# Kernel tuning notes

Measured on AMD Instinct MI355X. Metric: run time of the kernel, lower is better.

Reference implementation:

```python
import jax, jax.numpy as jnp
import numpy as np

N_LAYERS = 12
N_HEADS = 12
D_MODEL = 768
VOCAB = 50257
T_WIN = 1024
B, T = 4, 1024
STD = 0.02


def setup_inputs() -> dict:
    key = jax.random.key(0)
    ks = jax.random.split(key, 8)
    inp = jax.random.randint(ks[0], (B, T), 0, VOCAB)
    target = jax.random.randint(ks[1], (B, T), 0, VOCAB)
    wte = jax.random.normal(ks[2], (VOCAB, D_MODEL), jnp.float32) * STD
    wpe = jax.random.normal(ks[3], (T_WIN, D_MODEL), jnp.float32) * STD
    attn_w = jax.random.normal(ks[4], (N_LAYERS, D_MODEL, 3 * D_MODEL), jnp.float32) * STD
    proj_w = jax.random.normal(ks[5], (N_LAYERS, D_MODEL, D_MODEL), jnp.float32) * STD
    fc_w = jax.random.normal(ks[6], (N_LAYERS, D_MODEL, 4 * D_MODEL), jnp.float32) * STD
    fc2_w = jax.random.normal(ks[7], (N_LAYERS, 4 * D_MODEL, D_MODEL), jnp.float32) * STD
    return {
        'inp': inp, 'target': target, 'wte': wte, 'wpe': wpe,
        'ln1_w': jnp.ones((N_LAYERS, D_MODEL), jnp.float32),
        'ln1_b': jnp.zeros((N_LAYERS, D_MODEL), jnp.float32),
        'attn_w': attn_w,
        'attn_b': jnp.zeros((N_LAYERS, 3 * D_MODEL), jnp.float32),
        'proj_w': proj_w,
        'proj_b': jnp.zeros((N_LAYERS, D_MODEL), jnp.float32),
        'ln2_w': jnp.ones((N_LAYERS, D_MODEL), jnp.float32),
        'ln2_b': jnp.zeros((N_LAYERS, D_MODEL), jnp.float32),
        'fc_w': fc_w,
        'fc_b': jnp.zeros((N_LAYERS, 4 * D_MODEL), jnp.float32),
        'fc2_w': fc2_w,
        'fc2_b': jnp.zeros((N_LAYERS, D_MODEL), jnp.float32),
        'lnf_w': jnp.ones((D_MODEL,), jnp.float32),
        'lnf_b': jnp.zeros((D_MODEL,), jnp.float32),
    }


def _layernorm(x, w, b, eps=1e-5):
    mu = jnp.mean(x, axis=-1, keepdims=True)
    var = jnp.var(x, axis=-1, keepdims=True)
    return (x - mu) * jax.lax.rsqrt(var + eps) * w + b


def _attention(x, w_qkv, b_qkv, w_proj, b_proj):
    b, t, c = x.shape
    hd = c // N_HEADS
    qkv = x @ w_qkv + b_qkv                      # [B,T,3C]
    q, k, v = jnp.split(qkv, 3, axis=-1)
    # [B,H,T,hd]
    q = q.reshape(b, t, N_HEADS, hd).transpose(0, 2, 1, 3)
    k = k.reshape(b, t, N_HEADS, hd).transpose(0, 2, 1, 3)
    v = v.reshape(b, t, N_HEADS, hd).transpose(0, 2, 1, 3)
    scores = jnp.einsum('bhqd,bhkd->bhqk', q, k) / jnp.sqrt(jnp.float32(hd))
    causal = jnp.tril(jnp.ones((t, t), bool))
    scores = jnp.where(causal[None, None], scores, -jnp.inf)
    w = jax.nn.softmax(scores, axis=-1)          # dropout p=0 (eval)
    ctx = jnp.einsum('bhqk,bhkd->bhqd', w, v)
    ctx = ctx.transpose(0, 2, 1, 3).reshape(b, t, c)
    return ctx @ w_proj + b_proj


def reference(inp, target, wte, wpe, ln1_w, ln1_b, attn_w, attn_b, proj_w, proj_b,
              ln2_w, ln2_b, fc_w, fc_b, fc2_w, fc2_b, lnf_w, lnf_b):
    b, t = inp.shape
    x = wte[inp] + wpe[:t][None]                 # [B,T,C]
    for i in range(N_LAYERS):
        x = x + _attention(_layernorm(x, ln1_w[i], ln1_b[i]),
                           attn_w[i], attn_b[i], proj_w[i], proj_b[i])
        h = _layernorm(x, ln2_w[i], ln2_b[i])
        h = jax.nn.gelu(h @ fc_w[i] + fc_b[i], approximate=True)
        x = x + (h @ fc2_w[i] + fc2_b[i])
    x = _layernorm(x, lnf_w, lnf_b)
    logits = x @ wte.T                            # tied lm_head, no bias
    logp = jax.nn.log_softmax(logits, axis=-1)
    nll = -jnp.take_along_axis(logp, target[..., None], axis=-1)[..., 0]
    loss = jnp.mean(nll)
    return logits, loss
```

## Files before the change

kernel.cpp:

```cpp
#include <hip/hip_runtime.h>
#include <hip/hip_bf16.h>
#include <cmath>

#define NLAYERS 12
#define NHEADS  12
#define DM      768
#define VOCAB   50257
#define TSEQ    1024
#define BT      4096
#define NCHUNK  786

typedef __attribute__((ext_vector_type(4))) float f32x4;
typedef __attribute__((ext_vector_type(8))) short bf16x8;

typedef __hip_bfloat16 bf16;

#define MFMA16(a, b, c) __builtin_amdgcn_mfma_f32_16x16x32_bf16(a, b, c, 0, 0, 0)

__device__ __forceinline__ void gload16(const void* g, void* l) {
    __builtin_amdgcn_global_load_lds(
        (const __attribute__((address_space(1))) void*)g,
        (__attribute__((address_space(3))) void*)l, 16, 0, 0);
}

__device__ __forceinline__ float gelu_tanh(float v) {
    float u = 0.7978845608028654f * (v + 0.044715f * v * v * v);
    return 0.5f * v * (1.0f + tanhf(u));
}

__device__ __forceinline__ short f2bf(float f) {
    bf16 h = (bf16)f;
    return *reinterpret_cast<short*>(&h);
}

struct ushort4s { short a, b, c, d; };

__global__ void transpose_bf16_kernel(const float* __restrict__ in, bf16* __restrict__ out,
                                      int K, int N) {
    __shared__ float tile[32][33];
    size_t lofs = (size_t)blockIdx.z * K * N;
    int k0 = blockIdx.y * 32, n0 = blockIdx.x * 32;
    int tx = threadIdx.x, ty = threadIdx.y;
#pragma unroll
    for (int i = 0; i < 32; i += 8)
        tile[ty + i][tx] = in[lofs + (size_t)(k0 + ty + i) * N + n0 + tx];
    __syncthreads();
#pragma unroll
    for (int i = 0; i < 32; i += 8)
        out[lofs + (size_t)(n0 + ty + i) * K + k0 + tx] = (bf16)tile[tx][ty + i];
}

__global__ void tobf16_kernel(const float* __restrict__ in, bf16* __restrict__ out, size_t n) {
    size_t i = (size_t)blockIdx.x * 256 + threadIdx.x;
    if (i < n) out[i] = (bf16)in[i];
}

__global__ void embed_kernel(const int* __restrict__ inp, const float* __restrict__ wte,
                             const float* __restrict__ wpe, float* __restrict__ x) {
    int idx = blockIdx.x * 256 + threadIdx.x;
    int m = idx / (DM / 4), c4 = idx % (DM / 4);
    int tok = inp[m];
    int t = m & (TSEQ - 1);
    float4 a = reinterpret_cast<const float4*>(wte)[(size_t)tok * (DM / 4) + c4];
    float4 b = reinterpret_cast<const float4*>(wpe)[(size_t)t * (DM / 4) + c4];
    float4 o = {a.x + b.x, a.y + b.y, a.z + b.z, a.w + b.w};
    reinterpret_cast<float4*>(x)[idx] = o;
}

__global__ __launch_bounds__(256) void ln_kernel(const float* __restrict__ x,
                                                 const float* __restrict__ w,
                                                 const float* __restrict__ b,
                                                 bf16* __restrict__ y) {
    int row = blockIdx.x, tid = threadIdx.x;
    const float4* xr = reinterpret_cast<const float4*>(x + (size_t)row * DM);
    float4 v = {0.f, 0.f, 0.f, 0.f};
    float s = 0.f, q = 0.f;
    if (tid < 192) {
        v = xr[tid];
        s = v.x + v.y + v.z + v.w;
        q = v.x * v.x + v.y * v.y + v.z * v.z + v.w * v.w;
    }
#pragma unroll
    for (int o = 1; o < 64; o <<= 1) { s += __shfl_xor(s, o); q += __shfl_xor(q, o); }
    __shared__ float ss[4], qq[4];
    if ((tid & 63) == 0) { ss[tid >> 6] = s; qq[tid >> 6] = q; }
    __syncthreads();
    s = ss[0] + ss[1] + ss[2] + ss[3];
    q = qq[0] + qq[1] + qq[2] + qq[3];
    float mu  = s * (1.0f / DM);
    float var = q * (1.0f / DM) - mu * mu;
    float inv = rsqrtf(var + 1e-5f);
    if (tid < 192) {
        float4 wv = reinterpret_cast<const float4*>(w)[tid];
        float4 bv = reinterpret_cast<const float4*>(b)[tid];
        ushort4s o;
        o.a = f2bf((v.x - mu) * inv * wv.x + bv.x);
        o.b = f2bf((v.y - mu) * inv * wv.y + bv.y);
        o.c = f2bf((v.z - mu) * inv * wv.z + bv.z);
        o.d = f2bf((v.w - mu) * inv * wv.w + bv.w);
        *reinterpret_cast<ushort4s*>(y + (size_t)row * DM + tid * 4) = o;
    }
}

#define GF_GELU    1
#define GF_OBF16   2
#define GF_CLAMP   4
#define GF_PARTIAL 8
#define GF_SWZ     16

template<int FLAGS, int TAG>
__global__ __launch_bounds__(256) void gemm_k(
    const bf16* __restrict__ A, const bf16* __restrict__ Bt,
    const float* __restrict__ bias, const float* __restrict__ resid,
    void* __restrict__ C, float2* __restrict__ partials,
    int M, int N, int K) {
    __shared__ short ldsA[2][128 * 32];
    __shared__ short ldsB[2][128 * 32];
    int tid = threadIdx.x;
    int lane = tid & 63, w = tid >> 6;
    int wm = w >> 1, wn = w & 1;
    int r = lane & 15, kq = lane >> 4;

    int bm, bn;
    if (FLAGS & GF_SWZ) {
        int bid = blockIdx.x;
        int q = gridDim.x >> 3;
        int swz = (bid & 7) * q + (bid >> 3);
        int mblocks = M >> 7;
        bm = (swz % mblocks) * 128;
        bn = (swz / mblocks) * 128;
    } else {
        bm = blockIdx.x * 128;
        bn = blockIdx.y * 128;
    }

    f32x4 acc[4][4] = {};

    auto stage = [&](int buf, int k0) {
#pragma unroll
        for (int i = 0; i < 2; ++i) {
            int chunk = i * 256 + tid;
            int row = chunk >> 2;
            int gs = (chunk & 3) ^ ((row >> 1) & 3);
            const bf16* ga = A + (size_t)(bm + row) * K + k0 + gs * 8;
            gload16(ga, &ldsA[buf][(i * 256 + w * 64) * 8]);
            int brow = bn + row;
            if (FLAGS & GF_CLAMP) brow = min(brow, N - 1);
            const bf16* gb = Bt + (size_t)brow * K + k0 + gs * 8;
            gload16(gb, &ldsB[buf][(i * 256 + w * 64) * 8]);
        }
    };
    auto compute = [&](int buf) {
        bf16x8 af[4], bfr[4];
#pragma unroll
        for (int m = 0; m < 4; ++m) {
            int row = wm * 64 + m * 16 + r;
            af[m] = *reinterpret_cast<bf16x8*>(&ldsA[buf][row * 32 + (kq ^ ((row >> 1) & 3)) * 8]);
        }
#pragma unroll
        for (int n = 0; n < 4; ++n) {
            int row = wn * 64 + n * 16 + r;
            bfr[n] = *reinterpret_cast<bf16x8*>(&ldsB[buf][row * 32 + (kq ^ ((row >> 1) & 3)) * 8]);
        }
#pragma unroll
        for (int m = 0; m < 4; ++m)
#pragma unroll
            for (int n = 0; n < 4; ++n)
                acc[m][n] = MFMA16(af[m], bfr[n], acc[m][n]);
    };

    stage(0, 0);
    __syncthreads();
    int buf = 0;
    for (int k0 = 32; k0 < K; k0 += 32) {
        stage(buf ^ 1, k0);
        compute(buf);
        __syncthreads();
        buf ^= 1;
    }
    compute(buf);

    int row0 = bm + wm * 64, col0 = bn + wn * 64;
#pragma unroll
    for (int m = 0; m < 4; ++m) {
#pragma unroll
        for (int n = 0; n < 4; ++n) {
            int col = col0 + n * 16 + r;
            if (col < N) {
#pragma unroll
                for (int rr = 0; rr < 4; ++rr) {
                    int row = row0 + m * 16 + kq * 4 + rr;
                    float v = acc[m][n][rr];
                    if (bias) v += bias[col];
                    if (FLAGS & GF_GELU) v = gelu_tanh(v);
                    if (resid) v += resid[(size_t)row * N + col];
                    if (FLAGS & GF_OBF16) ((bf16*)C)[(size_t)row * N + col] = (bf16)v;
                    else                  ((float*)C)[(size_t)row * N + col] = v;
                }
            }
        }
    }

    if (FLAGS & GF_PARTIAL) {
        int chunk = (bn >> 6) + wn;
#pragma unroll
        for (int m = 0; m < 4; ++m) {
#pragma unroll
            for (int rr = 0; rr < 4; ++rr) {
                float vals[4], mx = -INFINITY;
#pragma unroll
                for (int n = 0; n < 4; ++n) {
                    int col = col0 + n * 16 + r;
                    float v = (col < N) ? acc[m][n][rr] : -INFINITY;
                    vals[n] = v;
                    mx = fmaxf(mx, v);
                }
#pragma unroll
                for (int o = 1; o < 16; o <<= 1) mx = fmaxf(mx, __shfl_xor(mx, o));
                float sum = 0.f;
#pragma unroll
                for (int n = 0; n < 4; ++n)
                    if (vals[n] > -INFINITY) sum += __expf(vals[n] - mx);
#pragma unroll
                for (int o = 1; o < 16; o <<= 1) sum += __shfl_xor(sum, o);
                if (r == 0) {
                    int row = row0 + m * 16 + kq * 4 + rr;
                    partials[(size_t)row * NCHUNK + chunk] = make_float2(mx, sum);
                }
            }
        }
    }
}

__global__ __launch_bounds__(256) void flash_attn_kernel(const bf16* __restrict__ qkv,
                                                         bf16* __restrict__ ctx) {
    __shared__ short Ks[128 * 64];
    __shared__ short Vt[64][132];
    __shared__ short Ps[4][16][132];

    int tid = threadIdx.x, lane = tid & 63, w = tid >> 6;
    int r = lane & 15, kq = lane >> 4;
    int q0 = blockIdx.x * 64;
    int bh = blockIdx.y;
    int b = bh / NHEADS, h = bh % NHEADS;
    const int RS = 3 * DM;

    const bf16* qbase = qkv + (size_t)(b * TSEQ + q0 + w * 16 + r) * RS + h * 64;
    bf16x8 qf[2];
    qf[0] = *reinterpret_cast<const bf16x8*>(qbase + kq * 8);
    qf[1] = *reinterpret_cast<const bf16x8*>(qbase + 32 + kq * 8);

    f32x4 of[4] = {};
    float mrow[4] = {-INFINITY, -INFINITY, -INFINITY, -INFINITY};
    float lrow[4] = {};

    int ntiles = (blockIdx.x >> 1) + 1;
    for (int t = 0; t < ntiles; ++t) {
        int kv0 = t * 128;
        __syncthreads();
        const bf16* kbase = qkv + (size_t)(b * TSEQ + kv0) * RS + DM + h * 64;
#pragma unroll
        for (int i = 0; i < 4; ++i) {
            int chunk = i * 256 + tid;
            int row = chunk >> 3, cp = chunk & 7;
            int csrc = cp ^ (row & 7);
            gload16(kbase + (size_t)row * RS + csrc * 8, Ks + chunk * 8);
        }
        const bf16* vbase = qkv + (size_t)(b * TSEQ + kv0) * RS + 2 * DM + h * 64;
#pragma unroll
        for (int i = 0; i < 4; ++i) {
            int chunk = i * 256 + tid;
            int kv = chunk >> 3, d0 = (chunk & 7) * 8;
            bf16x8 v = *reinterpret_cast<const bf16x8*>(vbase + (size_t)kv * RS + d0);
#pragma unroll
            for (int j = 0; j < 8; ++j) Vt[d0 + j][kv] = ((short*)&v)[j];
        }
        __syncthreads();

        f32x4 sf[8];
#pragma unroll
        for (int n = 0; n < 8; ++n) sf[n] = (f32x4){0.f, 0.f, 0.f, 0.f};
        __builtin_amdgcn_s_setprio(1);
#pragma unroll
        for (int n = 0; n < 8; ++n) {
            int row = n * 16 + r;
#pragma unroll
            for (int kt = 0; kt < 2; ++kt) {
                int gran = (kt * 4 + kq) ^ (row & 7);
                bf16x8 kf = *reinterpret_cast<bf16x8*>(&Ks[row * 64 + gran * 8]);
                sf[n] = MFMA16(qf[kt], kf, sf[n]);
            }
        }
        __builtin_amdgcn_s_setprio(0);

        bool diag = (kv0 + 128 > q0);
        float alpha[4];
#pragma unroll
        for (int rr = 0; rr < 4; ++rr) {
            int qrow = q0 + w * 16 + kq * 4 + rr;
            float vals[8];
            float mx = mrow[rr];
#pragma unroll
            for (int n = 0; n < 8; ++n) {
                float v = sf[n][rr] * 0.125f;
                if (diag && (kv0 + n * 16 + r) > qrow) v = -INFINITY;
                vals[n] = v;
                mx = fmaxf(mx, v);
            }
#pragma unroll
            for (int o = 1; o < 16; o <<= 1) mx = fmaxf(mx, __shfl_xor(mx, o));
            float al = __expf(mrow[rr] - mx);
            float sum = 0.f;
#pragma unroll
            for (int n = 0; n < 8; ++n) {
                float p = __expf(vals[n] - mx);
                vals[n] = p;
                sum += p;
            }
#pragma unroll
            for (int o = 1; o < 16; o <<= 1) sum += __shfl_xor(sum, o);
            mrow[rr] = mx;
            lrow[rr] = lrow[rr] * al + sum;
            alpha[rr] = al;
#pragma unroll
            for (int n = 0; n < 8; ++n) Ps[w][kq * 4 + rr][n * 16 + r] = f2bf(vals[n]);
        }
#pragma unroll
        for (int n = 0; n < 4; ++n)
#pragma unroll
            for (int rr = 0; rr < 4; ++rr) of[n][rr] *= alpha[rr];

        __builtin_amdgcn_s_setprio(1);
#pragma unroll
        for (int kt = 0; kt < 4; ++kt) {
            bf16x8 pa = *reinterpret_cast<bf16x8*>(&Ps[w][r][kt * 32 + kq * 8]);
#pragma unroll
            for (int n = 0; n < 4; ++n) {
                bf16x8 vf = *reinterpret_cast<bf16x8*>(&Vt[n * 16 + r][kt * 32 + kq * 8]);
                of[n] = MFMA16(pa, vf, of[n]);
            }
        }
        __builtin_amdgcn_s_setprio(0);
    }

#pragma unroll
    for (int rr = 0; rr < 4; ++rr) {
        float inv = 1.0f / lrow[rr];
        int qrow = q0 + w * 16 + kq * 4 + rr;
        bf16* cb = ctx + (size_t)(b * TSEQ + qrow) * DM + h * 64;
#pragma unroll
        for (int n = 0; n < 4; ++n) cb[n * 16 + r] = (bf16)(of[n][rr] * inv);
    }
}

__global__ __launch_bounds__(256) void loss_reduce_kernel(const float2* __restrict__ partials,
                                                          const float* __restrict__ logits,
                                                          const int* __restrict__ target,
                                                          float* __restrict__ nll) {
    int row = blockIdx.x, tid = threadIdx.x;
    const float2* pr = partials + (size_t)row * NCHUNK;
    float m = -INFINITY, s = 0.f;
    for (int c = tid; c < NCHUNK; c += 256) {
        float2 p = pr[c];
        if (p.x > m) { s = s * __expf(m - p.x) + p.y; m = p.x; }
        else         { s += p.y * __expf(p.x - m); }
    }
    __shared__ float sm[256], ssum[256];
    sm[tid] = m; ssum[tid] = s; __syncthreads();
    for (int o = 128; o; o >>= 1) {
        if (tid < o) {
            float m2 = sm[tid + o], s2 = ssum[tid + o];
            float mm = fmaxf(sm[tid], m2);
            ssum[tid] = ssum[tid] * __expf(sm[tid] - mm) + s2 * __expf(m2 - mm);
            sm[tid] = mm;
        }
        __syncthreads();
    }
    if (tid == 0) {
        float lse = sm[0] + logf(ssum[0]);
        nll[row] = lse - logits[(size_t)row * VOCAB + target[row]];
    }
}

__global__ void loss2_kernel(const float* __restrict__ nll, float* __restrict__ loss) {
    int tid = threadIdx.x;
    float s = 0.f;
    for (int i = tid; i < BT; i += 1024) s += nll[i];
    __shared__ float r[1024];
    r[tid] = s; __syncthreads();
    for (int o = 512; o; o >>= 1) { if (tid < o) r[tid] += r[tid + o]; __syncthreads(); }
    if (tid == 0) *loss = r[0] * (1.0f / BT);
}

extern "C" void kernel_launch(void* const* d_in, const int* in_sizes, int n_in,
                              void* d_out, int out_size, void* d_ws, size_t ws_size,
                              hipStream_t stream) {
    const int*   inp    = (const int*)  d_in[0];
    const int*   target = (const int*)  d_in[1];
    const float* wte    = (const float*)d_in[2];
    const float* wpe    = (const float*)d_in[3];
    const float* ln1_w  = (const float*)d_in[4];
    const float* ln1_b  = (const float*)d_in[5];
    const float* attn_w = (const float*)d_in[6];
    const float* attn_b = (const float*)d_in[7];
    const float* proj_w = (const float*)d_in[8];
    const float* proj_b = (const float*)d_in[9];
    const float* ln2_w  = (const float*)d_in[10];
    const float* ln2_b  = (const float*)d_in[11];
    const float* fc_w   = (const float*)d_in[12];
    const float* fc_b   = (const float*)d_in[13];
    const float* fc2_w  = (const float*)d_in[14];
    const float* fc2_b  = (const float*)d_in[15];
    const float* lnf_w  = (const float*)d_in[16];
    const float* lnf_b  = (const float*)d_in[17];
    float* out = (float*)d_out;

    char* p = (char*)d_ws;
    auto alloc = [&](size_t bytes) { char* q = p; p += (bytes + 255) & ~(size_t)255; return q; };
    float* x     = (float*)alloc((size_t)BT * DM * 4);
    float* nll   = (float*)alloc((size_t)BT * 4);
    bf16*  qkvb  = (bf16*) alloc((size_t)BT * 3 * DM * 2);
    bf16*  tmpb  = (bf16*) alloc((size_t)BT * DM * 2);
    bf16*  ctxb  = (bf16*) alloc((size_t)BT * DM * 2);
    bf16*  hb    = (bf16*) alloc((size_t)BT * 4 * DM * 2);
    bf16*  wteb  = (bf16*) alloc((size_t)VOCAB * DM * 2);
    bf16*  wqkvT = (bf16*) alloc((size_t)NLAYERS * 3 * DM * DM * 2);
    bf16*  wprojT= (bf16*) alloc((size_t)NLAYERS * DM * DM * 2);
    bf16*  wfcT  = (bf16*) alloc((size_t)NLAYERS * 4 * DM * DM * 2);
    bf16*  wfc2T = (bf16*) alloc((size_t)NLAYERS * 4 * DM * DM * 2);
    float2* partials = (float2*)ctxb;

    dim3 tb(32, 8);
    transpose_bf16_kernel<<<dim3(3 * DM / 32, DM / 32, NLAYERS), tb, 0, stream>>>(attn_w, wqkvT, DM, 3 * DM);
    transpose_bf16_kernel<<<dim3(DM / 32, DM / 32, NLAYERS), tb, 0, stream>>>(proj_w, wprojT, DM, DM);
    transpose_bf16_kernel<<<dim3(4 * DM / 32, DM / 32, NLAYERS), tb, 0, stream>>>(fc_w, wfcT, DM, 4 * DM);
    transpose_bf16_kernel<<<dim3(DM / 32, 4 * DM / 32, NLAYERS), tb, 0, stream>>>(fc2_w, wfc2T, 4 * DM, DM);
    {
        size_t n = (size_t)VOCAB * DM;
        tobf16_kernel<<<(unsigned)((n + 255) / 256), 256, 0, stream>>>(wte, wteb, n);
    }

    embed_kernel<<<BT * DM / 4 / 256, 256, 0, stream>>>(inp, wte, wpe, x);

    for (int i = 0; i < NLAYERS; ++i) {
        ln_kernel<<<BT, 256, 0, stream>>>(x, ln1_w + i * DM, ln1_b + i * DM, tmpb);
        gemm_k<GF_OBF16, 0><<<dim3(BT / 128, 3 * DM / 128), 256, 0, stream>>>(
            tmpb, wqkvT + (size_t)i * 3 * DM * DM, attn_b + i * 3 * DM, nullptr,
            qkvb, nullptr, BT, 3 * DM, DM);
        flash_attn_kernel<<<dim3(TSEQ / 64, 4 * NHEADS), 256, 0, stream>>>(qkvb, ctxb);
        gemm_k<0, 1><<<dim3(BT / 128, DM / 128), 256, 0, stream>>>(
            ctxb, wprojT + (size_t)i * DM * DM, proj_b + i * DM, x,
            x, nullptr, BT, DM, DM);
        ln_kernel<<<BT, 256, 0, stream>>>(x, ln2_w + i * DM, ln2_b + i * DM, tmpb);
        gemm_k<GF_GELU | GF_OBF16, 2><<<dim3(BT / 128, 4 * DM / 128), 256, 0, stream>>>(
            tmpb, wfcT + (size_t)i * 4 * DM * DM, fc_b + i * 4 * DM, nullptr,
            hb, nullptr, BT, 4 * DM, DM);
        gemm_k<0, 3><<<dim3(BT / 128, DM / 128), 256, 0, stream>>>(
            hb, wfc2T + (size_t)i * 4 * DM * DM, fc2_b + i * DM, x,
            x, nullptr, BT, DM, 4 * DM);
    }

    ln_kernel<<<BT, 256, 0, stream>>>(x, lnf_w, lnf_b, tmpb);
    {
        int nwg = (BT / 128) * ((VOCAB + 127) / 128);
        gemm_k<GF_CLAMP | GF_PARTIAL | GF_SWZ, 4><<<nwg, 256, 0, stream>>>(
            tmpb, wteb, nullptr, nullptr, out, partials, BT, VOCAB, DM);
    }
    loss_reduce_kernel<<<BT, 256, 0, stream>>>(partials, out, target, nll);
    loss2_kernel<<<1, 1024, 0, stream>>>(nll, out + (size_t)out_size - 1);
}
```

Baseline: 4.411 ms.

## Add 256x256-tile triple-buffered GEMM kernel for QKV, FC and LM-head

Introduces a 512-thread GEMM kernel with 256x256 output tiles, 8x4 MFMA accumulators per wave and a three-stage LDS pipeline driven by vmcnt waits. It is used for the QKV, FC1 and tied LM-head GEMMs, while the narrow proj and FC2 GEMMs stay on the 128-tile kernel. The larger tile raises operand reuse and cuts global/LDS traffic per FLOP. In exchange, the grid shrinks to 48-192 workgroups for the layer GEMMs, which risks underfilling the GPU's CUs, and the LM-head grid swizzle is removed. A chunk bound check guards the partial-softmax writes for the padded last tile.

Measured after the change: 4.618 ms. 4.7% more time.

```diff
diff --git a/kernel.cpp b/kernel.cpp
--- a/kernel.cpp
+++ b/kernel.cpp
@@ -106,7 +106,6 @@
 #define GF_OBF16   2
 #define GF_CLAMP   4
 #define GF_PARTIAL 8
-#define GF_SWZ     16
 
 template<int FLAGS, int TAG>
 __global__ __launch_bounds__(256) void gemm_k(
@@ -120,19 +119,7 @@
     int lane = tid & 63, w = tid >> 6;
     int wm = w >> 1, wn = w & 1;
     int r = lane & 15, kq = lane >> 4;
-
-    int bm, bn;
-    if (FLAGS & GF_SWZ) {
-        int bid = blockIdx.x;
-        int q = gridDim.x >> 3;
-        int swz = (bid & 7) * q + (bid >> 3);
-        int mblocks = M >> 7;
-        bm = (swz % mblocks) * 128;
-        bn = (swz / mblocks) * 128;
-    } else {
-        bm = blockIdx.x * 128;
-        bn = blockIdx.y * 128;
-    }
+    int bm = blockIdx.x * 128, bn = blockIdx.y * 128;
 
     f32x4 acc[4][4] = {};
 
@@ -200,32 +187,116 @@
             }
         }
     }
+}
+
+template<int FLAGS, int TAG>
+__global__ __launch_bounds__(512, 1) void gemm256_k(
+    const bf16* __restrict__ A, const bf16* __restrict__ Bt,
+    const float* __restrict__ bias, const float* __restrict__ resid,
+    void* __restrict__ C, float2* __restrict__ partials,
+    int M, int N, int K) {
+    __shared__ short lds[3][2][256 * 32];
+    int tid = threadIdx.x;
+    int lane = tid & 63, w = tid >> 6;
+    int wm = w >> 2, wn = w & 3;
+    int r = lane & 15, kq = lane >> 4;
+    int bm = blockIdx.x * 256, bn = blockIdx.y * 256;
+
+    f32x4 acc[8][4] = {};
+
+    auto stage = [&](int buf, int kt) {
+        int k0 = kt * 32;
+#pragma unroll
+        for (int i = 0; i < 2; ++i) {
+            int chunk = i * 512 + tid;
+            int row = chunk >> 2;
+            int gs = (chunk & 3) ^ ((row >> 1) & 3);
+            gload16(A + (size_t)(bm + row) * K + k0 + gs * 8,
+                    &lds[buf][0][(i * 512 + w * 64) * 8]);
+            int brow = bn + row;
+            if (FLAGS & GF_CLAMP) brow = min(brow, N - 1);
+            gload16(Bt + (size_t)brow * K + k0 + gs * 8,
+                    &lds[buf][1][(i * 512 + w * 64) * 8]);
+        }
+    };
+    auto compute = [&](int buf) {
+        bf16x8 bfr[4];
+#pragma unroll
+        for (int n = 0; n < 4; ++n) {
+            int row = wn * 64 + n * 16 + r;
+            bfr[n] = *reinterpret_cast<bf16x8*>(&lds[buf][1][row * 32 + (kq ^ ((row >> 1) & 3)) * 8]);
+        }
+#pragma unroll
+        for (int m = 0; m < 8; ++m) {
+            int row = wm * 128 + m * 16 + r;
+            bf16x8 af = *reinterpret_cast<bf16x8*>(&lds[buf][0][row * 32 + (kq ^ ((row >> 1) & 3)) * 8]);
+#pragma unroll
+            for (int n = 0; n < 4; ++n)
+                acc[m][n] = MFMA16(af, bfr[n], acc[m][n]);
+        }
+    };
+
+    const int NT = K / 32;
+    stage(0, 0);
+    stage(1, 1);
+    asm volatile("s_waitcnt vmcnt(4)" ::: "memory");
+    __builtin_amdgcn_s_barrier();
+    for (int kt = 0; kt < NT; ++kt) {
+        if (kt + 2 < NT) stage((kt + 2) % 3, kt + 2);
+        compute(kt % 3);
+        if (kt + 2 < NT) asm volatile("s_waitcnt vmcnt(4)" ::: "memory");
+        else             asm volatile("s_waitcnt vmcnt(0)" ::: "memory");
+        __builtin_amdgcn_s_barrier();
+    }
+
+    int row0 = bm + wm * 128, col0 = bn + wn * 64;
+#pragma unroll
+    for (int m = 0; m < 8; ++m) {
+#pragma unroll
+        for (int n = 0; n < 4; ++n) {
+            int col = col0 + n * 16 + r;
+            if (col < N) {
+#pragma unroll
+                for (int rr = 0; rr < 4; ++rr) {
+                    int row = row0 + m * 16 + kq * 4 + rr;
+                    float v = acc[m][n][rr];
+                    if (bias) v += bias[col];
+                    if (FLAGS & GF_GELU) v = gelu_tanh(v);
+                    if (resid) v += resid[(size_t)row * N + col];
+                    if (FLAGS & GF_OBF16) ((bf16*)C)[(size_t)row * N + col] = (bf16)v;
+                    else                  ((float*)C)[(size_t)row * N + col] = v;
+                }
+            }
+        }
+    }
 
     if (FLAGS & GF_PARTIAL) {
         int chunk = (bn >> 6) + wn;
-#pragma unroll
-        for (int m = 0; m < 4; ++m) {
-#pragma unroll
-            for (int rr = 0; rr < 4; ++rr) {
-                float vals[4], mx = -INFINITY;
-#pragma unroll
-                for (int n = 0; n < 4; ++n) {
-                    int col = col0 + n * 16 + r;
-                    float v = (col < N) ? acc[m][n][rr] : -INFINITY;
-                    vals[n] = v;
-                    mx = fmaxf(mx, v);
-                }
-#pragma unroll
-                for (int o = 1; o < 16; o <<= 1) mx = fmaxf(mx, __shfl_xor(mx, o));
-                float sum = 0.f;
-#pragma unroll
-                for (int n = 0; n < 4; ++n)
-                    if (vals[n] > -INFINITY) sum += __expf(vals[n] - mx);
-#pragma unroll
-                for (int o = 1; o < 16; o <<= 1) sum += __shfl_xor(sum, o);
-                if (r == 0) {
-                    int row = row0 + m * 16 + kq * 4 + rr;
-                    partials[(size_t)row * NCHUNK + chunk] = make_float2(mx, sum);
+        if (chunk < NCHUNK) {
+#pragma unroll
+            for (int m = 0; m < 8; ++m) {
+#pragma unroll
+                for (int rr = 0; rr < 4; ++rr) {
+                    float vals[4], mx = -INFINITY;
+#pragma unroll
+                    for (int n = 0; n < 4; ++n) {
+                        int col = col0 + n * 16 + r;
+                        float v = (col < N) ? acc[m][n][rr] : -INFINITY;
+                        vals[n] = v;
+                        mx = fmaxf(mx, v);
+                    }
+#pragma unroll
+                    for (int o = 1; o < 16; o <<= 1) mx = fmaxf(mx, __shfl_xor(mx, o));
+                    float sum = 0.f;
+#pragma unroll
+                    for (int n = 0; n < 4; ++n)
+                        if (vals[n] > -INFINITY) sum += __expf(vals[n] - mx);
+#pragma unroll
+                    for (int o = 1; o < 16; o <<= 1) sum += __shfl_xor(sum, o);
+                    if (r == 0) {
+                        int row = row0 + m * 16 + kq * 4 + rr;
+                        partials[(size_t)row * NCHUNK + chunk] = make_float2(mx, sum);
+                    }
                 }
             }
         }
@@ -444,7 +515,7 @@
 
     for (int i = 0; i < NLAYERS; ++i) {
         ln_kernel<<<BT, 256, 0, stream>>>(x, ln1_w + i * DM, ln1_b + i * DM, tmpb);
-        gemm_k<GF_OBF16, 0><<<dim3(BT / 128, 3 * DM / 128), 256, 0, stream>>>(
+        gemm256_k<GF_OBF16, 0><<<dim3(BT / 256, 3 * DM / 256), 512, 0, stream>>>(
             tmpb, wqkvT + (size_t)i * 3 * DM * DM, attn_b + i * 3 * DM, nullptr,
             qkvb, nullptr, BT, 3 * DM, DM);
         flash_attn_kernel<<<dim3(TSEQ / 64, 4 * NHEADS), 256, 0, stream>>>(qkvb, ctxb);
@@ -452,7 +523,7 @@
             ctxb, wprojT + (size_t)i * DM * DM, proj_b + i * DM, x,
             x, nullptr, BT, DM, DM);
         ln_kernel<<<BT, 256, 0, stream>>>(x, ln2_w + i * DM, ln2_b + i * DM, tmpb);
-        gemm_k<GF_GELU | GF_OBF16, 2><<<dim3(BT / 128, 4 * DM / 128), 256, 0, stream>>>(
+        gemm256_k<GF_GELU | GF_OBF16, 2><<<dim3(BT / 256, 4 * DM / 256), 512, 0, stream>>>(
             tmpb, wfcT + (size_t)i * 4 * DM * DM, fc_b + i * 4 * DM, nullptr,
             hb, nullptr, BT, 4 * DM, DM);
         gemm_k<0, 3><<<dim3(BT / 128, DM / 128), 256, 0, stream>>>(
@@ -461,11 +532,8 @@
     }
 
     ln_kernel<<<BT, 256, 0, stream>>>(x, lnf_w, lnf_b, tmpb);
-    {
-        int nwg = (BT / 128) * ((VOCAB + 127) / 128);
-        gemm_k<GF_CLAMP | GF_PARTIAL | GF_SWZ, 4><<<nwg, 256, 0, stream>>>(
-            tmpb, wteb, nullptr, nullptr, out, partials, BT, VOCAB, DM);
-    }
+    gemm256_k<GF_CLAMP | GF_PARTIAL, 4><<<dim3(BT / 256, (VOCAB + 255) / 256), 512, 0, stream>>>(
+        tmpb, wteb, nullptr, nullptr, out, partials, BT, VOCAB, DM);
     loss_reduce_kernel<<<BT, 256, 0, stream>>>(partials, out, target, nll);
     loss2_kernel<<<1, 1024, 0, stream>>>(nll, out + (size_t)out_size - 1);
 }
```
